# Performance work log

Hardware: AMD Instinct MI355X
Metric: run time of the kernel (lower is better)

The kernel has to match this reference:

```python
import jax, jax.numpy as jnp
import numpy as np

N_NODES = 4096  # nodes per graph (output1 reshaped to [-1, N_NODES])


def setup_inputs() -> dict:
    key = jax.random.key(0)
    ks = jax.random.split(key, 10)
    total_nodes = 64 * N_NODES          # 64 graphs of 4096 nodes
    n_edges = total_nodes * 8           # avg degree 8 lattice-like graph
    n_hidden = 128
    return {
        "node_features": jax.random.normal(ks[0], (total_nodes, 1), jnp.float32),
        "src": jax.random.randint(ks[1], (n_edges,), 0, total_nodes, jnp.int32),
        "dst": jax.random.randint(ks[2], (n_edges,), 0, total_nodes, jnp.int32),
        "w_self1": jax.random.normal(ks[3], (1, n_hidden), jnp.float32) * 0.5,
        "w_neigh1": jax.random.normal(ks[4], (1, n_hidden), jnp.float32) * 0.5,
        "b1": jnp.zeros((n_hidden,), jnp.float32),
        "w_self2": jax.random.normal(ks[5], (n_hidden, 1), jnp.float32) * (1.0 / np.sqrt(n_hidden)),
        "w_neigh2": jax.random.normal(ks[6], (n_hidden, 1), jnp.float32) * (1.0 / np.sqrt(n_hidden)),
        "b2": jnp.zeros((1,), jnp.float32),
        "w3": jax.random.normal(ks[7], (N_NODES, N_NODES), jnp.float32) * (1.0 / np.sqrt(N_NODES)),
        "b3": jnp.zeros((N_NODES,), jnp.float32),
    }


def _sage_mean(feat, src, dst, w_self, w_neigh, b, num_nodes):
    # gather source-node features along edges, mean-reduce at destination
    agg = jax.ops.segment_sum(feat[src], dst, num_segments=num_nodes)
    deg = jax.ops.segment_sum(jnp.ones((src.shape[0], 1), feat.dtype), dst,
                              num_segments=num_nodes)
    h_neigh = agg / jnp.maximum(deg, 1.0)
    return feat @ w_self + h_neigh @ w_neigh + b


def reference(node_features, src, dst, w_self1, w_neigh1, b1,
              w_self2, w_neigh2, b2, w3, b3):
    n = node_features.shape[0]
    h1 = jnp.tanh(_sage_mean(node_features, src, dst, w_self1, w_neigh1, b1, n))
    out1 = _sage_mean(h1, src, dst, w_self2, w_neigh2, b2, n)
    output1 = out1.reshape(-1, N_NODES)          # [batch, n_nodes]
    h2 = jnp.tanh(output1)
    output2 = h2 @ w3 + b3
    return (output1, output2)
```

## Files before the change

### kernel.cpp

```cpp
#include <hip/hip_runtime.h>


#define NTOT (64 * 4096)
#define NHID 128
#define GK   4096
#define KCH  256
#define KCHUNKS 16
#define NBINS 128
#define BSZ   2048
#define BSH   11
#define CAP   17408
#define NSL   4
#define SCB   256

typedef unsigned int u32;

__device__ __forceinline__ float fast_tanh(float x) {
    float ax = fabsf(x);
    float t  = __expf(-2.0f * ax);
    float r  = (1.0f - t) / (1.0f + t);
    return copysignf(r, x);
}


__global__ void __launch_bounds__(1024) scatter_x(const int* __restrict__ src,
                                                  const int* __restrict__ dst,
                                                  int n_edges,
                                                  int* __restrict__ edge_cnt,
                                                  u32* __restrict__ packed) {
    __shared__ int lc[NBINS];
    __shared__ int lbase[NBINS];
    int t = threadIdx.x;
    if (t < NBINS) lc[t] = 0;
    __syncthreads();
    int per = (n_edges + gridDim.x - 1) / gridDim.x;
    int e0 = blockIdx.x * per;
    int e1 = min(e0 + per, n_edges);
    for (int e = e0 + t; e < e1; e += 1024)
        atomicAdd(&lc[dst[e] >> BSH], 1);
    __syncthreads();
    if (t < NBINS) {
        lbase[t] = atomicAdd(&edge_cnt[t], lc[t]);
        lc[t] = 0;
    }
    __syncthreads();
    for (int e = e0 + t; e < e1; e += 1024) {
        int d = dst[e];
        int b = d >> BSH;
        int pos = lbase[b] + atomicAdd(&lc[b], 1);
        if (pos < CAP)
            packed[(size_t)b * CAP + pos] =
                ((u32)(d & (BSZ - 1)) << 18) | (u32)src[e];
    }
}

__global__ void __launch_bounds__(1024) agg1_x(const u32* __restrict__ packed,
                                               const int* __restrict__ edge_cnt,
                                               const float* __restrict__ nf,
                                               float* __restrict__ part1) {
    __shared__ float lsum[BSZ];
    __shared__ float lcnt[BSZ];
    int t = threadIdx.x;
    int b = blockIdx.x, s = blockIdx.y;
    for (int i = t; i < BSZ; i += 1024) { lsum[i] = 0.0f; lcnt[i] = 0.0f; }
    __syncthreads();
    int en  = min(edge_cnt[b], CAP);
    int per = (en + NSL - 1) / NSL;
    int e0  = s * per;
    int e1  = min(e0 + per, en);
    const u32* pk = packed + (size_t)b * CAP;
    for (int e = e0 + t; e < e1; e += 1024) {
        u32 p = pk[e];
        int local = (int)(p >> 18);
        atomicAdd(&lsum[local], nf[p & 0x3FFFFu]);
        atomicAdd(&lcnt[local], 1.0f);
    }
    __syncthreads();
    float* dp = part1 + ((size_t)(b * NSL + s) * 2) * BSZ;
    for (int i = t; i < BSZ; i += 1024) { dp[i] = lsum[i]; dp[BSZ + i] = lcnt[i]; }
}

__global__ void node1_x(const float* __restrict__ nf, const float* __restrict__ part1,
                        const float* __restrict__ w_s1, const float* __restrict__ w_n1,
                        const float* __restrict__ bb1,
                        const float* __restrict__ w_s2, const float* __restrict__ w_n2,
                        float* __restrict__ degf, float* __restrict__ selfp,
                        float* __restrict__ sp) {
    __shared__ float lws1[NHID], lwn1[NHID], lb1[NHID], lws2[NHID], lwn2[NHID];
    int tid = threadIdx.x;
    if (tid < NHID) {
        lws1[tid] = w_s1[tid];
        lwn1[tid] = w_n1[tid];
        lb1[tid]  = bb1[tid];
        lws2[tid] = w_s2[tid];
        lwn2[tid] = w_n2[tid];
    }
    __syncthreads();
    int v = blockIdx.x * blockDim.x + tid;
    int b = v >> BSH, local = v & (BSZ - 1);
    float sum = 0.0f, cf = 0.0f;
#pragma unroll
    for (int s = 0; s < NSL; ++s) {
        const float* dp = part1 + ((size_t)(b * NSL + s) * 2) * BSZ;
        sum += dp[local];
        cf  += dp[BSZ + local];
    }
    float hn = sum / fmaxf(cf, 1.0f);
    float f = nf[v];
    float a = 0.0f, s2 = 0.0f;
#pragma unroll 8
    for (int j = 0; j < NHID; ++j) {
        float t = fast_tanh(fmaf(f, lws1[j], fmaf(hn, lwn1[j], lb1[j])));
        a  = fmaf(t, lws2[j], a);
        s2 = fmaf(t, lwn2[j], s2);
    }
    degf[v]  = cf;
    selfp[v] = a;
    sp[v]    = s2;
}

__global__ void __launch_bounds__(1024) agg2_x(const u32* __restrict__ packed,
                                               const int* __restrict__ edge_cnt,
                                               const float* __restrict__ spv,
                                               float* __restrict__ part2) {
    __shared__ float lsum[BSZ];
    int t = threadIdx.x;
    int b = blockIdx.x, s = blockIdx.y;
    for (int i = t; i < BSZ; i += 1024) lsum[i] = 0.0f;
    __syncthreads();
    int en  = min(edge_cnt[b], CAP);
    int per = (en + NSL - 1) / NSL;
    int e0  = s * per;
    int e1  = min(e0 + per, en);
    const u32* pk = packed + (size_t)b * CAP;
    for (int e = e0 + t; e < e1; e += 1024) {
        u32 p = pk[e];
        atomicAdd(&lsum[p >> 18], spv[p & 0x3FFFFu]);
    }
    __syncthreads();
    float* dp = part2 + (size_t)(b * NSL + s) * BSZ;
    for (int i = t; i < BSZ; i += 1024) dp[i] = lsum[i];
}

__global__ void node2_x(const float* __restrict__ selfp, const float* __restrict__ part2,
                        const float* __restrict__ degf, const float* __restrict__ b2p,
                        float* __restrict__ out1, float* __restrict__ h2t) {
    int v = blockIdx.x * blockDim.x + threadIdx.x;
    int b = v >> BSH, local = v & (BSZ - 1);
    float agg2 = 0.0f;
#pragma unroll
    for (int s = 0; s < NSL; ++s)
        agg2 += part2[(size_t)(b * NSL + s) * BSZ + local];
    float o = selfp[v] + agg2 / fmaxf(degf[v], 1.0f) + b2p[0];
    out1[v] = o;
    int r = v >> 12;
    int k = v & 4095;
    h2t[k * 64 + r] = fast_tanh(o);
}

__global__ void __launch_bounds__(512, 4) gemm_x(const float* __restrict__ h2t,
                                                 const float* __restrict__ w3,
                                                 float* __restrict__ Cpart) {
    int lane = threadIdx.x & 63;
    int wv   = threadIdx.x >> 6;
    int col  = blockIdx.x * 64 + lane;
    int k0   = blockIdx.y * KCH;
    int row0 = __builtin_amdgcn_readfirstlane(wv * 8);

    const float* Ap = h2t + (size_t)k0 * 64 + row0;
    const float* wp = w3 + (size_t)k0 * GK + col;

    float acc[8];
#pragma unroll
    for (int r = 0; r < 8; ++r) acc[r] = 0.0f;

    float bvA[8], bvB[8];
    float avA[8], avB[8];

#pragma unroll
    for (int j = 0; j < 8; ++j) bvA[j] = wp[(size_t)j * GK];
#pragma unroll
    for (int r = 0; r < 8; ++r) avA[r] = Ap[r];

    for (int kk = 0; kk < KCH; kk += 16) {
#pragma unroll
        for (int j = 0; j < 8; ++j) bvB[j] = wp[(size_t)(kk + 8 + j) * GK];
#pragma unroll
        for (int j = 0; j < 8; ++j) {
            const float* An = Ap + (size_t)(kk + j + 1) * 64;
            if ((j & 1) == 0) {
#pragma unroll
                for (int r = 0; r < 8; ++r) avB[r] = An[r];
                float b = bvA[j];
#pragma unroll
                for (int r = 0; r < 8; ++r) acc[r] = fmaf(avA[r], b, acc[r]);
            } else {
#pragma unroll
                for (int r = 0; r < 8; ++r) avA[r] = An[r];
                float b = bvA[j];
#pragma unroll
                for (int r = 0; r < 8; ++r) acc[r] = fmaf(avB[r], b, acc[r]);
            }
        }
        if (kk + 16 < KCH) {
#pragma unroll
            for (int j = 0; j < 8; ++j) bvA[j] = wp[(size_t)(kk + 16 + j) * GK];
        }
#pragma unroll
        for (int j = 0; j < 8; ++j) {
            int kn = kk + 8 + j + 1;
            if (kn > KCH - 1) kn = KCH - 1;
            const float* An = Ap + (size_t)kn * 64;
            if ((j & 1) == 0) {
#pragma unroll
                for (int r = 0; r < 8; ++r) avB[r] = An[r];
                float b = bvB[j];
#pragma unroll
                for (int r = 0; r < 8; ++r) acc[r] = fmaf(avA[r], b, acc[r]);
            } else {
#pragma unroll
                for (int r = 0; r < 8; ++r) avA[r] = An[r];
                float b = bvB[j];
#pragma unroll
                for (int r = 0; r < 8; ++r) acc[r] = fmaf(avB[r], b, acc[r]);
            }
        }
    }

    float* Cp = Cpart + (size_t)blockIdx.y * NTOT + (size_t)row0 * GK + col;
#pragma unroll
    for (int r = 0; r < 8; ++r) Cp[(size_t)r * GK] = acc[r];
}

__global__ void reduce_x(const float4* __restrict__ Cpart, const float4* __restrict__ b3v,
                         float4* __restrict__ out2) {
    int v = blockIdx.x * blockDim.x + threadIdx.x;
    float4 s = b3v[v & 1023];
#pragma unroll
    for (int kc = 0; kc < KCHUNKS; ++kc) {
        float4 c = Cpart[(size_t)kc * (NTOT / 4) + v];
        s.x += c.x; s.y += c.y; s.z += c.z; s.w += c.w;
    }
    out2[v] = s;
}


__global__ void edge_pass1_f(const int* __restrict__ src, const int* __restrict__ dst,
                             const float* __restrict__ nf, float* __restrict__ agg,
                             float* __restrict__ deg, int n_edges) {
    int e = blockIdx.x * blockDim.x + threadIdx.x;
    if (e >= n_edges) return;
    int s = src[e], d = dst[e];
    atomicAdd(&agg[d], nf[s]);
    atomicAdd(&deg[d], 1.0f);
}

__global__ void node1_f(const float* __restrict__ nf, float* s0,
                        const float* __restrict__ deg,
                        const float* __restrict__ w_s1, const float* __restrict__ w_n1,
                        const float* __restrict__ bb1,
                        const float* __restrict__ w_s2, const float* __restrict__ w_n2,
                        float* __restrict__ sp) {
    __shared__ float lws1[NHID], lwn1[NHID], lb1[NHID], lws2[NHID], lwn2[NHID];
    int tid = threadIdx.x;
    if (tid < NHID) {
        lws1[tid] = w_s1[tid];
        lwn1[tid] = w_n1[tid];
        lb1[tid]  = bb1[tid];
        lws2[tid] = w_s2[tid];
        lwn2[tid] = w_n2[tid];
    }
    __syncthreads();
    int v = blockIdx.x * blockDim.x + tid;
    float f  = nf[v];
    float hn = s0[v] / fmaxf(deg[v], 1.0f);
    float a = 0.0f, s = 0.0f;
#pragma unroll 8
    for (int j = 0; j < NHID; ++j) {
        float t = fast_tanh(fmaf(f, lws1[j], fmaf(hn, lwn1[j], lb1[j])));
        a = fmaf(t, lws2[j], a);
        s = fmaf(t, lwn2[j], s);
    }
    s0[v] = a;
    sp[v] = s;
}

__global__ void edge_pass2_f(const int* __restrict__ src, const int* __restrict__ dst,
                             const float* __restrict__ sp, float* __restrict__ agg2,
                             int n_edges) {
    int e = blockIdx.x * blockDim.x + threadIdx.x;
    if (e >= n_edges) return;
    atomicAdd(&agg2[dst[e]], sp[src[e]]);
}

__global__ void node2_f(const float* __restrict__ s0, const float* __restrict__ agg2,
                        const float* __restrict__ deg, const float* __restrict__ b2p,
                        const float* __restrict__ b3p,
                        float* __restrict__ out1, float* __restrict__ h2t,
                        float* __restrict__ out2) {
    int v = blockIdx.x * blockDim.x + threadIdx.x;
    float o = s0[v] + agg2[v] / fmaxf(deg[v], 1.0f) + b2p[0];
    out1[v] = o;
    int r = v >> 12;
    int k = v & 4095;
    h2t[k * 64 + r] = fast_tanh(o);
    out2[v] = b3p[v & 4095];
}

__global__ void __launch_bounds__(256) gemm_f(const float* __restrict__ h2t,
                                              const float* __restrict__ w3,
                                              float* __restrict__ out2) {
    int n  = blockIdx.x * 256 + threadIdx.x;
    int k0 = blockIdx.y * KCH;
    float acc[64];
#pragma unroll
    for (int r = 0; r < 64; ++r) acc[r] = 0.0f;
    for (int k = k0; k < k0 + KCH; ++k) {
        float bv = w3[(size_t)k * GK + n];
        const float* Ak = h2t + k * 64;
#pragma unroll
        for (int r = 0; r < 64; ++r) acc[r] = fmaf(Ak[r], bv, acc[r]);
    }
#pragma unroll
    for (int r = 0; r < 64; ++r) atomicAdd(&out2[r * GK + n], acc[r]);
}


extern "C" void kernel_launch(void* const* d_in, const int* in_sizes, int n_in,
                              void* d_out, int out_size, void* d_ws, size_t ws_size,
                              hipStream_t stream) {
    const float* nf  = (const float*)d_in[0];
    const int*   src = (const int*)d_in[1];
    const int*   dst = (const int*)d_in[2];
    const float* ws1 = (const float*)d_in[3];
    const float* wn1 = (const float*)d_in[4];
    const float* b1  = (const float*)d_in[5];
    const float* ws2 = (const float*)d_in[6];
    const float* wn2 = (const float*)d_in[7];
    const float* b2  = (const float*)d_in[8];
    const float* w3  = (const float*)d_in[9];
    const float* b3  = (const float*)d_in[10];
    float* out1 = (float*)d_out;
    float* out2 = (float*)d_out + NTOT;

    int n_edges = in_sizes[1];
    int eb = (n_edges + 255) / 256;

    if (ws_size >= (size_t)20 * 1024 * 1024 && n_edges <= (1 << 21)) {
        char*  base     = (char*)d_ws;
        u32*   packed   = (u32*)base;
        float* part     = (float*)(base + 8912896);
        float* degf     = (float*)(base + 17301504);
        float* selfp    = (float*)(base + 18350080);
        float* spbuf    = (float*)(base + 19398656);
        int*   edge_cnt = (int*)(base + 20447232);
        float* h2t      = spbuf;
        float* Cpart    = (float*)base;

        (void)hipMemsetAsync(edge_cnt, 0, NBINS * sizeof(int), stream);
        scatter_x<<<SCB, 1024, 0, stream>>>(src, dst, n_edges, edge_cnt, packed);
        agg1_x<<<dim3(NBINS, NSL), 1024, 0, stream>>>(packed, edge_cnt, nf, part);
        node1_x<<<NTOT / 256, 256, 0, stream>>>(nf, part, ws1, wn1, b1, ws2, wn2,
                                                degf, selfp, spbuf);
        agg2_x<<<dim3(NBINS, NSL), 1024, 0, stream>>>(packed, edge_cnt, spbuf, part);
        node2_x<<<NTOT / 256, 256, 0, stream>>>(selfp, part, degf, b2, out1, h2t);
        gemm_x<<<dim3(GK / 64, KCHUNKS), 512, 0, stream>>>(h2t, w3, Cpart);
        reduce_x<<<NTOT / 4 / 256, 256, 0, stream>>>((const float4*)Cpart,
                                                     (const float4*)b3, (float4*)out2);
    } else {
        float* ws = (float*)d_ws;
        float* S0 = ws;
        float* S1 = ws + 1 * NTOT;
        float* S2 = ws + 2 * NTOT;
        float* S3 = ws + 3 * NTOT;

        (void)hipMemsetAsync(S0, 0, (size_t)3 * NTOT * sizeof(float), stream);
        edge_pass1_f<<<eb, 256, 0, stream>>>(src, dst, nf, S0, S1, n_edges);
        node1_f<<<NTOT / 256, 256, 0, stream>>>(nf, S0, S1, ws1, wn1, b1, ws2, wn2, S3);
        edge_pass2_f<<<eb, 256, 0, stream>>>(src, dst, S3, S2, n_edges);
        node2_f<<<NTOT / 256, 256, 0, stream>>>(S0, S2, S1, b2, b3, out1, S3, out2);
        gemm_f<<<dim3(GK / 256, KCHUNKS), 256, 0, stream>>>(S3, w3, out2);
    }
}
```

Baseline: 244.7 us.

## Widen GEMM tile to two columns per thread and register-cache scatter edges

The w3 GEMM now computes two adjacent output columns per thread. It loads w3 as float2 and reuses each h2t value across two FMAs, halving A-operand loads per FMA and the block count. The scatter kernel keeps each thread's eight dst/src values in registers between the counting and placement passes, so the edge arrays are read from global memory only once. The register caching assumes at most 8192 edges per block, which the n_edges guard ensures. The extra accumulator registers could lower GEMM occupancy.

```diff
diff --git a/kernel.cpp b/kernel.cpp
--- a/kernel.cpp
+++ b/kernel.cpp
@@ -36,21 +36,33 @@
     int per = (n_edges + gridDim.x - 1) / gridDim.x;
     int e0 = blockIdx.x * per;
     int e1 = min(e0 + per, n_edges);
-    for (int e = e0 + t; e < e1; e += 1024)
-        atomicAdd(&lc[dst[e] >> BSH], 1);
+
+    int dreg[8], sreg[8];
+#pragma unroll
+    for (int i = 0; i < 8; ++i) {
+        int e = e0 + t + i * 1024;
+        bool ok = e < e1;
+        int d = ok ? dst[e] : -1;
+        dreg[i] = d;
+        sreg[i] = ok ? src[e] : 0;
+        if (ok) atomicAdd(&lc[d >> BSH], 1);
+    }
     __syncthreads();
     if (t < NBINS) {
         lbase[t] = atomicAdd(&edge_cnt[t], lc[t]);
         lc[t] = 0;
     }
     __syncthreads();
-    for (int e = e0 + t; e < e1; e += 1024) {
-        int d = dst[e];
-        int b = d >> BSH;
-        int pos = lbase[b] + atomicAdd(&lc[b], 1);
-        if (pos < CAP)
-            packed[(size_t)b * CAP + pos] =
-                ((u32)(d & (BSZ - 1)) << 18) | (u32)src[e];
+#pragma unroll
+    for (int i = 0; i < 8; ++i) {
+        int d = dreg[i];
+        if (d >= 0) {
+            int b = d >> BSH;
+            int pos = lbase[b] + atomicAdd(&lc[b], 1);
+            if (pos < CAP)
+                packed[(size_t)b * CAP + pos] =
+                    ((u32)(d & (BSZ - 1)) << 18) | (u32)sreg[i];
+        }
     }
 }
 
@@ -163,73 +175,85 @@
                                                  float* __restrict__ Cpart) {
     int lane = threadIdx.x & 63;
     int wv   = threadIdx.x >> 6;
-    int col  = blockIdx.x * 64 + lane;
+    int colb = blockIdx.x * 128 + lane * 2;
     int k0   = blockIdx.y * KCH;
     int row0 = __builtin_amdgcn_readfirstlane(wv * 8);
 
     const float* Ap = h2t + (size_t)k0 * 64 + row0;
-    const float* wp = w3 + (size_t)k0 * GK + col;
-
-    float acc[8];
-#pragma unroll
-    for (int r = 0; r < 8; ++r) acc[r] = 0.0f;
-
-    float bvA[8], bvB[8];
-    float avA[8], avB[8];
-
-#pragma unroll
-    for (int j = 0; j < 8; ++j) bvA[j] = wp[(size_t)j * GK];
+    const float* wp = w3 + (size_t)k0 * GK + colb;
+
+    float2 acc[8];
+#pragma unroll
+    for (int r = 0; r < 8; ++r) { acc[r].x = 0.0f; acc[r].y = 0.0f; }
+
+    float2 bvA[8], bvB[8];
+    float  avA[8], avB[8];
+
+#pragma unroll
+    for (int j = 0; j < 8; ++j) bvA[j] = *(const float2*)(wp + (size_t)j * GK);
 #pragma unroll
     for (int r = 0; r < 8; ++r) avA[r] = Ap[r];
 
     for (int kk = 0; kk < KCH; kk += 16) {
 #pragma unroll
-        for (int j = 0; j < 8; ++j) bvB[j] = wp[(size_t)(kk + 8 + j) * GK];
+        for (int j = 0; j < 8; ++j)
+            bvB[j] = *(const float2*)(wp + (size_t)(kk + 8 + j) * GK);
 #pragma unroll
         for (int j = 0; j < 8; ++j) {
             const float* An = Ap + (size_t)(kk + j + 1) * 64;
+            float2 b = bvA[j];
             if ((j & 1) == 0) {
 #pragma unroll
                 for (int r = 0; r < 8; ++r) avB[r] = An[r];
-                float b = bvA[j];
-#pragma unroll
-                for (int r = 0; r < 8; ++r) acc[r] = fmaf(avA[r], b, acc[r]);
+#pragma unroll
+                for (int r = 0; r < 8; ++r) {
+                    acc[r].x = fmaf(avA[r], b.x, acc[r].x);
+                    acc[r].y = fmaf(avA[r], b.y, acc[r].y);
+                }
             } else {
 #pragma unroll
                 for (int r = 0; r < 8; ++r) avA[r] = An[r];
-                float b = bvA[j];
-#pragma unroll
-                for (int r = 0; r < 8; ++r) acc[r] = fmaf(avB[r], b, acc[r]);
+#pragma unroll
+                for (int r = 0; r < 8; ++r) {
+                    acc[r].x = fmaf(avB[r], b.x, acc[r].x);
+                    acc[r].y = fmaf(avB[r], b.y, acc[r].y);
+                }
             }
         }
         if (kk + 16 < KCH) {
 #pragma unroll
-            for (int j = 0; j < 8; ++j) bvA[j] = wp[(size_t)(kk + 16 + j) * GK];
+            for (int j = 0; j < 8; ++j)
+                bvA[j] = *(const float2*)(wp + (size_t)(kk + 16 + j) * GK);
         }
 #pragma unroll
         for (int j = 0; j < 8; ++j) {
             int kn = kk + 8 + j + 1;
             if (kn > KCH - 1) kn = KCH - 1;
             const float* An = Ap + (size_t)kn * 64;
+            float2 b = bvB[j];
             if ((j & 1) == 0) {
 #pragma unroll
                 for (int r = 0; r < 8; ++r) avB[r] = An[r];
-                float b = bvB[j];
-#pragma unroll
-                for (int r = 0; r < 8; ++r) acc[r] = fmaf(avA[r], b, acc[r]);
+#pragma unroll
+                for (int r = 0; r < 8; ++r) {
+                    acc[r].x = fmaf(avA[r], b.x, acc[r].x);
+                    acc[r].y = fmaf(avA[r], b.y, acc[r].y);
+                }
             } else {
 #pragma unroll
                 for (int r = 0; r < 8; ++r) avA[r] = An[r];
-                float b = bvB[j];
-#pragma unroll
-                for (int r = 0; r < 8; ++r) acc[r] = fmaf(avB[r], b, acc[r]);
+#pragma unroll
+                for (int r = 0; r < 8; ++r) {
+                    acc[r].x = fmaf(avB[r], b.x, acc[r].x);
+                    acc[r].y = fmaf(avB[r], b.y, acc[r].y);
+                }
             }
         }
     }
 
-    float* Cp = Cpart + (size_t)blockIdx.y * NTOT + (size_t)row0 * GK + col;
-#pragma unroll
-    for (int r = 0; r < 8; ++r) Cp[(size_t)r * GK] = acc[r];
+    float* Cp = Cpart + (size_t)blockIdx.y * NTOT + (size_t)row0 * GK + colb;
+#pragma unroll
+    for (int r = 0; r < 8; ++r) *(float2*)(Cp + (size_t)r * GK) = acc[r];
 }
 
 __global__ void reduce_x(const float4* __restrict__ Cpart, const float4* __restrict__ b3v,
@@ -364,7 +388,7 @@
                                                 degf, selfp, spbuf);
         agg2_x<<<dim3(NBINS, NSL), 1024, 0, stream>>>(packed, edge_cnt, spbuf, part);
         node2_x<<<NTOT / 256, 256, 0, stream>>>(selfp, part, degf, b2, out1, h2t);
-        gemm_x<<<dim3(GK / 64, KCHUNKS), 512, 0, stream>>>(h2t, w3, Cpart);
+        gemm_x<<<dim3(GK / 128, KCHUNKS), 512, 0, stream>>>(h2t, w3, Cpart);
         reduce_x<<<NTOT / 4 / 256, 256, 0, stream>>>((const float4*)Cpart,
                                                      (const float4*)b3, (float4*)out2);
     } else {
```

Result: no change. 247.2 us (+1.0%).

## Fuse per-bin aggregation with node updates and shrink destination bins

Applied to the files above, without the earlier changes.

Destination bins drop from 2048 to 1024 nodes, which doubles the bin count. With 1024 threads per block, each block can own one bin outright and apply the node-level layer math straight from shared memory. This removes the partial-sum slices and the separate node1/node2 kernels, saving two launches and the global round trip of the partial buffers. The scatter kernel now keeps dst/src in registers so edges are read once instead of twice. The trade-off is fewer blocks per aggregation pass (256 instead of 512), and a fixed limit of 8 edges per thread in scatter, which holds only for the current edge count.

```diff
diff --git a/kernel.cpp b/kernel.cpp
--- a/kernel.cpp
+++ b/kernel.cpp
@@ -6,11 +6,10 @@
 #define GK   4096
 #define KCH  256
 #define KCHUNKS 16
-#define NBINS 128
-#define BSZ   2048
-#define BSH   11
-#define CAP   17408
-#define NSL   4
+#define NBINS 256
+#define BSZ   1024
+#define BSH   10
+#define CAP   8960
 #define SCB   256
 
 typedef unsigned int u32;
@@ -36,122 +35,109 @@
     int per = (n_edges + gridDim.x - 1) / gridDim.x;
     int e0 = blockIdx.x * per;
     int e1 = min(e0 + per, n_edges);
-    for (int e = e0 + t; e < e1; e += 1024)
-        atomicAdd(&lc[dst[e] >> BSH], 1);
+
+    int dreg[8], sreg[8];
+#pragma unroll
+    for (int i = 0; i < 8; ++i) {
+        int e = e0 + t + i * 1024;
+        bool ok = e < e1;
+        int d = ok ? dst[e] : -1;
+        dreg[i] = d;
+        sreg[i] = ok ? src[e] : 0;
+        if (ok) atomicAdd(&lc[d >> BSH], 1);
+    }
     __syncthreads();
     if (t < NBINS) {
         lbase[t] = atomicAdd(&edge_cnt[t], lc[t]);
         lc[t] = 0;
     }
     __syncthreads();
-    for (int e = e0 + t; e < e1; e += 1024) {
-        int d = dst[e];
-        int b = d >> BSH;
-        int pos = lbase[b] + atomicAdd(&lc[b], 1);
-        if (pos < CAP)
-            packed[(size_t)b * CAP + pos] =
-                ((u32)(d & (BSZ - 1)) << 18) | (u32)src[e];
-    }
-}
-
-__global__ void __launch_bounds__(1024) agg1_x(const u32* __restrict__ packed,
+#pragma unroll
+    for (int i = 0; i < 8; ++i) {
+        int d = dreg[i];
+        if (d >= 0) {
+            int b = d >> BSH;
+            int pos = lbase[b] + atomicAdd(&lc[b], 1);
+            if (pos < CAP)
+                packed[(size_t)b * CAP + pos] =
+                    ((u32)(d & (BSZ - 1)) << 18) | (u32)sreg[i];
+        }
+    }
+}
+
+__global__ void __launch_bounds__(1024) agn1_x(const u32* __restrict__ packed,
                                                const int* __restrict__ edge_cnt,
                                                const float* __restrict__ nf,
-                                               float* __restrict__ part1) {
+                                               const float* __restrict__ w_s1,
+                                               const float* __restrict__ w_n1,
+                                               const float* __restrict__ bb1,
+                                               const float* __restrict__ w_s2,
+                                               const float* __restrict__ w_n2,
+                                               float* __restrict__ degf,
+                                               float* __restrict__ selfp,
+                                               float* __restrict__ sp) {
     __shared__ float lsum[BSZ];
     __shared__ float lcnt[BSZ];
+    __shared__ float lws1[NHID], lwn1[NHID], lb1[NHID], lws2[NHID], lwn2[NHID];
     int t = threadIdx.x;
-    int b = blockIdx.x, s = blockIdx.y;
-    for (int i = t; i < BSZ; i += 1024) { lsum[i] = 0.0f; lcnt[i] = 0.0f; }
-    __syncthreads();
-    int en  = min(edge_cnt[b], CAP);
-    int per = (en + NSL - 1) / NSL;
-    int e0  = s * per;
-    int e1  = min(e0 + per, en);
+    int b = blockIdx.x;
+    lsum[t] = 0.0f;
+    lcnt[t] = 0.0f;
+    if (t < NHID) {
+        lws1[t] = w_s1[t];
+        lwn1[t] = w_n1[t];
+        lb1[t]  = bb1[t];
+        lws2[t] = w_s2[t];
+        lwn2[t] = w_n2[t];
+    }
+    __syncthreads();
+    int en = min(edge_cnt[b], CAP);
     const u32* pk = packed + (size_t)b * CAP;
-    for (int e = e0 + t; e < e1; e += 1024) {
+    for (int e = t; e < en; e += 1024) {
         u32 p = pk[e];
         int local = (int)(p >> 18);
         atomicAdd(&lsum[local], nf[p & 0x3FFFFu]);
         atomicAdd(&lcnt[local], 1.0f);
     }
     __syncthreads();
-    float* dp = part1 + ((size_t)(b * NSL + s) * 2) * BSZ;
-    for (int i = t; i < BSZ; i += 1024) { dp[i] = lsum[i]; dp[BSZ + i] = lcnt[i]; }
-}
-
-__global__ void node1_x(const float* __restrict__ nf, const float* __restrict__ part1,
-                        const float* __restrict__ w_s1, const float* __restrict__ w_n1,
-                        const float* __restrict__ bb1,
-                        const float* __restrict__ w_s2, const float* __restrict__ w_n2,
-                        float* __restrict__ degf, float* __restrict__ selfp,
-                        float* __restrict__ sp) {
-    __shared__ float lws1[NHID], lwn1[NHID], lb1[NHID], lws2[NHID], lwn2[NHID];
-    int tid = threadIdx.x;
-    if (tid < NHID) {
-        lws1[tid] = w_s1[tid];
-        lwn1[tid] = w_n1[tid];
-        lb1[tid]  = bb1[tid];
-        lws2[tid] = w_s2[tid];
-        lwn2[tid] = w_n2[tid];
-    }
-    __syncthreads();
-    int v = blockIdx.x * blockDim.x + tid;
-    int b = v >> BSH, local = v & (BSZ - 1);
-    float sum = 0.0f, cf = 0.0f;
-#pragma unroll
-    for (int s = 0; s < NSL; ++s) {
-        const float* dp = part1 + ((size_t)(b * NSL + s) * 2) * BSZ;
-        sum += dp[local];
-        cf  += dp[BSZ + local];
-    }
-    float hn = sum / fmaxf(cf, 1.0f);
-    float f = nf[v];
+    int v = b * BSZ + t;
+    float cf = lcnt[t];
+    float hn = lsum[t] / fmaxf(cf, 1.0f);
+    float f  = nf[v];
     float a = 0.0f, s2 = 0.0f;
 #pragma unroll 8
     for (int j = 0; j < NHID; ++j) {
-        float t = fast_tanh(fmaf(f, lws1[j], fmaf(hn, lwn1[j], lb1[j])));
-        a  = fmaf(t, lws2[j], a);
-        s2 = fmaf(t, lwn2[j], s2);
+        float th = fast_tanh(fmaf(f, lws1[j], fmaf(hn, lwn1[j], lb1[j])));
+        a  = fmaf(th, lws2[j], a);
+        s2 = fmaf(th, lwn2[j], s2);
     }
     degf[v]  = cf;
     selfp[v] = a;
     sp[v]    = s2;
 }
 
-__global__ void __launch_bounds__(1024) agg2_x(const u32* __restrict__ packed,
+__global__ void __launch_bounds__(1024) agn2_x(const u32* __restrict__ packed,
                                                const int* __restrict__ edge_cnt,
                                                const float* __restrict__ spv,
-                                               float* __restrict__ part2) {
+                                               const float* __restrict__ selfp,
+                                               const float* __restrict__ degf,
+                                               const float* __restrict__ b2p,
+                                               float* __restrict__ out1,
+                                               float* __restrict__ h2t) {
     __shared__ float lsum[BSZ];
     int t = threadIdx.x;
-    int b = blockIdx.x, s = blockIdx.y;
-    for (int i = t; i < BSZ; i += 1024) lsum[i] = 0.0f;
-    __syncthreads();
-    int en  = min(edge_cnt[b], CAP);
-    int per = (en + NSL - 1) / NSL;
-    int e0  = s * per;
-    int e1  = min(e0 + per, en);
+    int b = blockIdx.x;
+    lsum[t] = 0.0f;
+    __syncthreads();
+    int en = min(edge_cnt[b], CAP);
     const u32* pk = packed + (size_t)b * CAP;
-    for (int e = e0 + t; e < e1; e += 1024) {
+    for (int e = t; e < en; e += 1024) {
         u32 p = pk[e];
         atomicAdd(&lsum[p >> 18], spv[p & 0x3FFFFu]);
     }
     __syncthreads();
-    float* dp = part2 + (size_t)(b * NSL + s) * BSZ;
-    for (int i = t; i < BSZ; i += 1024) dp[i] = lsum[i];
-}
-
-__global__ void node2_x(const float* __restrict__ selfp, const float* __restrict__ part2,
-                        const float* __restrict__ degf, const float* __restrict__ b2p,
-                        float* __restrict__ out1, float* __restrict__ h2t) {
-    int v = blockIdx.x * blockDim.x + threadIdx.x;
-    int b = v >> BSH, local = v & (BSZ - 1);
-    float agg2 = 0.0f;
-#pragma unroll
-    for (int s = 0; s < NSL; ++s)
-        agg2 += part2[(size_t)(b * NSL + s) * BSZ + local];
-    float o = selfp[v] + agg2 / fmaxf(degf[v], 1.0f) + b2p[0];
+    int v = b * BSZ + t;
+    float o = selfp[v] + lsum[t] / fmaxf(degf[v], 1.0f) + b2p[0];
     out1[v] = o;
     int r = v >> 12;
     int k = v & 4095;
@@ -349,21 +335,19 @@
     if (ws_size >= (size_t)20 * 1024 * 1024 && n_edges <= (1 << 21)) {
         char*  base     = (char*)d_ws;
         u32*   packed   = (u32*)base;
-        float* part     = (float*)(base + 8912896);
-        float* degf     = (float*)(base + 17301504);
-        float* selfp    = (float*)(base + 18350080);
-        float* spbuf    = (float*)(base + 19398656);
-        int*   edge_cnt = (int*)(base + 20447232);
-        float* h2t      = spbuf;
+        float* degf     = (float*)(base + 10485760);
+        float* selfp    = (float*)(base + 11534336);
+        float* spbuf    = (float*)(base + 12582912);
+        float* h2t      = (float*)(base + 16777216);
+        int*   edge_cnt = (int*)(base + 17825792);
         float* Cpart    = (float*)base;
 
         (void)hipMemsetAsync(edge_cnt, 0, NBINS * sizeof(int), stream);
         scatter_x<<<SCB, 1024, 0, stream>>>(src, dst, n_edges, edge_cnt, packed);
-        agg1_x<<<dim3(NBINS, NSL), 1024, 0, stream>>>(packed, edge_cnt, nf, part);
-        node1_x<<<NTOT / 256, 256, 0, stream>>>(nf, part, ws1, wn1, b1, ws2, wn2,
-                                                degf, selfp, spbuf);
-        agg2_x<<<dim3(NBINS, NSL), 1024, 0, stream>>>(packed, edge_cnt, spbuf, part);
-        node2_x<<<NTOT / 256, 256, 0, stream>>>(selfp, part, degf, b2, out1, h2t);
+        agn1_x<<<NBINS, 1024, 0, stream>>>(packed, edge_cnt, nf, ws1, wn1, b1,
+                                           ws2, wn2, degf, selfp, spbuf);
+        agn2_x<<<NBINS, 1024, 0, stream>>>(packed, edge_cnt, spbuf, selfp, degf,
+                                           b2, out1, h2t);
         gemm_x<<<dim3(GK / 64, KCHUNKS), 512, 0, stream>>>(h2t, w3, Cpart);
         reduce_x<<<NTOT / 4 / 256, 256, 0, stream>>>((const float4*)Cpart,
                                                      (const float4*)b3, (float4*)out2);
```

Result: faster. 229.7 us (-6.1%).
